# Performance work log

Measured on AMD Instinct MI355X. Metric: run time of the kernel, lower is better.

## Reference

```python
import jax, jax.numpy as jnp
import numpy as np


def conv2d(x, w, b, pad):
    # NCHW conv, stride 1, symmetric padding
    out = jax.lax.conv_general_dilated(
        x, w, window_strides=(1, 1), padding=[(pad, pad), (pad, pad)],
        dimension_numbers=("NCHW", "OIHW", "NCHW"))
    return out + b[None, :, None, None]


def setup_inputs() -> dict:
    key = jax.random.key(0)
    ks = jax.random.split(key, 18)
    B, C, H, W = 4, 256, 64, 64
    Cq = C // 16  # 16
    Ck = C // 8   # 32
    s = 0.02
    return {
        "x": jax.random.normal(ks[0], (B, C, H, W), jnp.float32),
        "dw1_w": jax.random.normal(ks[1], (Cq, C, 7, 7), jnp.float32) * s,
        "dw1_b": jnp.zeros((Cq,), jnp.float32),
        "dw2_w": jax.random.normal(ks[2], (Cq, C, 11, 11), jnp.float32) * s,
        "dw2_b": jnp.zeros((Cq,), jnp.float32),
        "key_w": jax.random.normal(ks[3], (Ck, C, 1, 1), jnp.float32) * s,
        "key_b": jnp.zeros((Ck,), jnp.float32),
        "value_w": jax.random.normal(ks[4], (C, C, 1, 1), jnp.float32) * s,
        "value_b": jnp.zeros((C,), jnp.float32),
        "conv1_w": jax.random.normal(ks[5], (Cq, C, 3, 3), jnp.float32) * s,
        "conv1_b": jnp.zeros((Cq,), jnp.float32),
        "conv2_w": jax.random.normal(ks[6], (C, Cq, 3, 3), jnp.float32) * s,
        "conv2_b": jnp.zeros((C,), jnp.float32),
        "se_w": jax.random.normal(ks[7], (C, C, 1, 1), jnp.float32) * s,
        "se_b": jnp.zeros((C,), jnp.float32),
        "gamma1": jnp.zeros((1,), jnp.float32) + 0.1,  # nonzero so attention path is exercised
        "gamma2": jnp.zeros((1,), jnp.float32) + 0.1,
    }


def reference(x, dw1_w, dw1_b, dw2_w, dw2_b, key_w, key_b, value_w, value_b,
              conv1_w, conv1_b, conv2_w, conv2_b, se_w, se_b, gamma1, gamma2):
    B, C, H, W = x.shape
    HW = H * W
    # q: concat of 7x7 and 11x11 conv branches -> (B, HW, C//8)
    q = jnp.concatenate([conv2d(x, dw1_w, dw1_b, 3), conv2d(x, dw2_w, dw2_b, 5)], axis=1)
    q = q.reshape(B, -1, HW).transpose(0, 2, 1)
    # k: 1x1 conv -> (B, C//8, HW)
    k = conv2d(x, key_w, key_b, 0).reshape(B, -1, HW)
    # raw (unscaled) full spatial attention, softmax over last dim
    att = jax.nn.softmax(jnp.einsum("bnc,bcm->bnm", q, k), axis=-1)  # (B, HW, HW)
    v = conv2d(x, value_w, value_b, 0).reshape(B, C, HW)
    out = jnp.einsum("bcm,bnm->bcn", v, att).reshape(B, C, H, W)
    # local conv branch + channel attention (SE)
    y = conv2d(jax.nn.silu(conv2d(x, conv1_w, conv1_b, 1)), conv2_w, conv2_b, 1)
    pooled = jnp.mean(y, axis=(2, 3), keepdims=True)  # (B, C, 1, 1)
    se = y * jax.nn.sigmoid(conv2d(pooled, se_w, se_b, 0))
    return gamma1 * out + gamma2 * se + x
```

## Files before the change

kernel.cpp:

```cpp
#include <hip/hip_runtime.h>

typedef unsigned short u16;
typedef __bf16 bf16x8 __attribute__((ext_vector_type(8)));
typedef float f32x4 __attribute__((ext_vector_type(4)));
typedef float f32x16 __attribute__((ext_vector_type(16)));

#define MFMA16(A,B,C) __builtin_amdgcn_mfma_f32_16x16x32_bf16((A),(B),(C),0,0,0)
#define MFMA32(A,B,C) __builtin_amdgcn_mfma_f32_32x32x16_bf16((A),(B),(C),0,0,0)

__device__ __forceinline__ u16 f2b(float f){
  union { float f; unsigned u; } X; X.f = f;
  unsigned r = X.u + 0x7FFFu + ((X.u >> 16) & 1u);
  return (u16)(r >> 16);
}
__device__ __forceinline__ float b2f(u16 h){
  union { unsigned u; float f; } X; X.u = ((unsigned)h) << 16; return X.f;
}
__device__ __forceinline__ u16 f2b_trunc(float f){
  union { float f; unsigned u; } X; X.f = f;
  return (u16)(X.u >> 16);
}
__device__ __forceinline__ bf16x8 ld_frag(const u16* p){
  union { uint4 u; bf16x8 v; } U; U.u = *(const uint4*)p; return U.v;
}

__global__ __launch_bounds__(256) void k_prep_w(
    const float* __restrict__ dw1, const float* __restrict__ dw2,
    const float* __restrict__ cw1, const float* __restrict__ kw,
    const float* __restrict__ vw,  const float* __restrict__ cw2,
    u16* __restrict__ wB, u16* __restrict__ wC,
    u16* __restrict__ kwt, u16* __restrict__ vwt, u16* __restrict__ w2t){
  int i = blockIdx.x * 256 + threadIdx.x;
  const int NB = 991232, NC = 73728, NK = 8192, NV = 65536, N2 = 40960;
  if(i < NB){
    int tap = i >> 13, rem = i & 8191;
    int chunk = rem >> 9, r2 = rem & 511;
    int oc = r2 >> 4, ci = chunk*16 + (r2 & 15);
    int dy = tap / 11, dx = tap - dy*11;
    float v;
    if(oc < 16){
      v = (dy >= 2 && dy <= 8 && dx >= 2 && dx <= 8) ? dw1[(oc*256 + ci)*49 + (dy-2)*7 + (dx-2)] : 0.f;
    } else {
      v = dw2[((oc-16)*256 + ci)*121 + tap];
    }
    wB[i] = f2b(v);
    return;
  }
  i -= NB;
  if(i < NC){
    int tap = i >> 13, rem = i & 8191;
    int chunk = rem >> 9, r2 = rem & 511;
    int oc = r2 >> 4, ci = chunk*16 + (r2 & 15);
    wC[i] = (oc < 16) ? f2b(cw1[(oc*256 + ci)*9 + tap]) : (u16)0;
    return;
  }
  i -= NC;
  if(i < NK){ kwt[i] = f2b(kw[i]); return; }
  i -= NK;
  if(i < NV){ vwt[i] = f2b(vw[i]); return; }
  i -= NV;
  if(i < N2){
    int co = i/160, kk = i - co*160;
    int tap = kk >> 4, ci = kk & 15;
    w2t[i] = (tap < 9) ? f2b(cw2[co*144 + ci*9 + tap]) : (u16)0;
    return;
  }
}

__global__ __launch_bounds__(256) void k_prep_x(const float* __restrict__ x, u16* __restrict__ xp){
  __shared__ float tile[32][33];
  const int bid = blockIdx.x;
  const int b = bid >> 10, rem = bid & 1023;
  const int c0 = (rem >> 7) << 5, m0 = (rem & 127) << 5;
  const int t = threadIdx.x;
  { const int cg = t >> 5, mm = t & 31;
    #pragma unroll
    for(int i=0;i<4;i++)
      tile[cg*4+i][mm] = x[((size_t)(b*256 + c0 + cg*4 + i) << 12) + m0 + mm];
  }
  __syncthreads();
  { const int cp = (t & 15) << 1, mloc = t >> 4;
    #pragma unroll
    for(int half = 0; half < 2; ++half){
      const int ml = half*16 + mloc;
      const int m = m0 + ml;
      const int yy = (m >> 6) + 5, xx = (m & 63) + 5;
      const int ci = c0 + cp;
      const int chunk = ci >> 4, wi = ci & 15;
      u16 lo = f2b(tile[cp][ml]), hi = f2b(tile[cp+1][ml]);
      *(unsigned*)&xp[(((size_t)(b*16 + chunk)*74 + yy)*80 + xx)*16 + wi] = ((unsigned)hi << 16) | lo;
    }
  }
}

__global__ __launch_bounds__(256) void k_qconv(
    const u16* __restrict__ xp, const u16* __restrict__ wB, const u16* __restrict__ wC,
    u16* __restrict__ qp){
  __shared__ __align__(16) u16 buf[15360];
  const int bid = blockIdx.x;
  const int rg = bid & 31, b = (bid >> 5) & 3, kq = bid >> 7;
  const int y0 = rg << 1;
  const int t = threadIdx.x, wv = t >> 6, lane = t & 63;
  const int m = lane & 31, kh = lane >> 5;
  const int laneoff = m*16 + kh*8;
  const int r = wv & 1, xo = (wv >> 1) << 5;
  const f32x16 z16 = {0.f,0.f,0.f,0.f,0.f,0.f,0.f,0.f,0.f,0.f,0.f,0.f,0.f,0.f,0.f,0.f};
  f32x16 acc = z16, acc1 = z16;

  #pragma unroll 1
  for(int c = 0; c < 2; ++c){
    const int chunk = kq*2 + c;
    const uint4* src = (const uint4*)(xp + ((size_t)((b*16 + chunk)*74 + y0))*1280);
    __syncthreads();
    for(int e = t; e < 1920; e += 256){
      ((uint4*)buf)[(e & 1)*960 + (e >> 1)] = src[e];
    }
    __syncthreads();
    const u16* wBc = wB + chunk*512 + laneoff;
    const u16* wCc = wC + chunk*512 + laneoff;
    const u16* ap = buf + kh*7680 + (r*80 + xo + m)*8;
    #pragma unroll 1
    for(int dy = 0; dy < 11; ++dy){
      const u16* rowp = ap + dy*640;
      const u16* wrow = wBc + dy*11*8192;
      const bool in1y = (dy >= 4) & (dy <= 6);
      #pragma unroll
      for(int dx = 0; dx < 11; ++dx){
        bf16x8 A = ld_frag(rowp + dx*8);
        bf16x8 B = ld_frag(wrow + dx*8192);
        acc = MFMA32(A, B, acc);
        if(in1y && dx >= 4 && dx <= 6){
          bf16x8 B1 = ld_frag(wCc + ((dy-4)*3 + (dx-4))*8192);
          acc1 = MFMA32(A, B1, acc1);
        }
      }
    }
  }

  u16* qb = qp + ((size_t)kq*16384 + (b << 12) + (y0 + r)*64 + xo) * 48;
  #pragma unroll
  for(int reg = 0; reg < 16; ++reg){
    const int row = (reg & 3) + ((reg >> 2) << 3) + (kh << 2);
    qb[row*48 + m] = f2b(acc[reg]);
    if(m < 16) qb[row*48 + 32 + m] = f2b(acc1[reg]);
  }
}

__global__ __launch_bounds__(256) void k_qfin(
    const u16* __restrict__ qp, const float* __restrict__ b7,
    const float* __restrict__ b11, const float* __restrict__ b1,
    u16* __restrict__ q_t, u16* __restrict__ t1){
  const int t = threadIdx.x, wv = t >> 6, lane = t & 63;
  const int px = blockIdx.x*4 + wv;
  if(lane >= 48) return;
  const size_t off = (size_t)px*48 + lane;
  float s = 0.f;
  #pragma unroll
  for(int sp = 0; sp < 8; ++sp) s += b2f(qp[off + (size_t)sp*786432]);
  const float LOG2E = 1.44269504f;
  if(lane < 16){
    q_t[px*32 + lane] = f2b((s + b7[lane]) * LOG2E);
  } else if(lane < 32){
    q_t[px*32 + lane] = f2b((s + b11[lane - 16]) * LOG2E);
  } else {
    float v = s + b1[lane - 32];
    t1[px*16 + lane - 32] = f2b(v / (1.f + __expf(-v)));
  }
}

__global__ __launch_bounds__(256) void k_kv(
    const u16* __restrict__ xp, const u16* __restrict__ vwt, const u16* __restrict__ kwt,
    const float* __restrict__ vb, const float* __restrict__ kb,
    u16* __restrict__ vt, u16* __restrict__ k_t){
  const int bid = blockIdx.x;
  const int h = bid & 3, blk = (bid >> 2) & 63, b = bid >> 8;
  const int wv = threadIdx.x >> 6, lane = threadIdx.x & 63;
  const int col = lane & 15, quad = lane >> 4;
  const int m0 = (blk << 6) + (wv << 4);
  f32x4 z = {0.f,0.f,0.f,0.f};
  f32x4 av[4], ak[2];
  #pragma unroll
  for(int i=0;i<4;i++) av[i] = z;
  ak[0] = z; ak[1] = z;
  const int m = m0 + col;
  const int py = (m >> 6) + 5, pxx = (m & 63) + 5;
  #pragma unroll 1
  for(int ch = 0; ch < 8; ++ch){
    const int cio = ch*32 + quad*8;
    const int chunk = cio >> 4, wi = cio & 15;
    bf16x8 xf = ld_frag(xp + (((size_t)(b*16 + chunk)*74 + py)*80 + pxx)*16 + wi);
    #pragma unroll
    for(int ct2 = 0; ct2 < 4; ++ct2){
      bf16x8 wf = ld_frag(vwt + (((h*4 + ct2)*16 + col) << 8) + cio);
      av[ct2] = MFMA16(wf, xf, av[ct2]);
    }
    if(h == 0){
      #pragma unroll
      for(int kt = 0; kt < 2; ++kt){
        bf16x8 kf = ld_frag(kwt + ((kt*16 + col) << 8) + cio);
        ak[kt] = MFMA16(xf, kf, ak[kt]);
      }
    }
  }
  const int g = m0 >> 5, lo = (m0 & 31) + col;
  #pragma unroll
  for(int ct2 = 0; ct2 < 4; ++ct2){
    #pragma unroll
    for(int r = 0; r < 4; ++r){
      const int c = (h*4 + ct2)*16 + quad*4 + r;
      vt[((size_t)(b*128 + g)*256 + c)*32 + lo] = f2b(av[ct2][r] + vb[c]);
    }
  }
  if(h == 0){
    #pragma unroll
    for(int kt = 0; kt < 2; ++kt){
      #pragma unroll
      for(int r = 0; r < 4; ++r){
        const int mq = b*4096 + m0 + quad*4 + r;
        k_t[mq*32 + kt*16 + col] = f2b((ak[kt][r] + kb[kt*16 + col]) );
      }
    }
  }
}

__global__ __launch_bounds__(512) void k_attn(
    const u16* __restrict__ q_t, const u16* __restrict__ k_t,
    const u16* __restrict__ vt, u16* __restrict__ Op,
    float* __restrict__ lsav){
  __shared__ __align__(16) u16 P[2][128][72];
  __shared__ float lred[2][128];
  __shared__ float l_l[128];
  const int bid = blockIdx.x;
  const int q0 = (bid & 31) << 7, b = (bid >> 5) & 3, ks = bid >> 7;
  const int t = threadIdx.x, wv = t >> 6, lane = t & 63, col = lane & 15, quad = lane >> 4;
  const int qp2 = wv & 3, kh2 = wv >> 2;
  const int cb = wv << 5;
  const bf16x8 qf0 = ld_frag(q_t + (size_t)(b*4096 + q0 + (qp2*2+0)*16 + col) * 32 + quad*8);
  const bf16x8 qf1 = ld_frag(q_t + (size_t)(b*4096 + q0 + (qp2*2+1)*16 + col) * 32 + quad*8);
  const f32x4 z = {0.f,0.f,0.f,0.f};
  f32x4 acc[8][2];
  #pragma unroll
  for(int qq=0;qq<8;qq++){ acc[qq][0] = z; acc[qq][1] = z; }
  float lp0[4] = {0.f,0.f,0.f,0.f};
  float lp1[4] = {0.f,0.f,0.f,0.f};
  const u16* kbase = k_t + (size_t)(b*4096) * 32;
  const u16* vbase = vt + (size_t)(b*128) * 8192;

  const int ktEnd = ks*16 + 16;
  for(int kt = ks*16; kt < ktEnd; ++kt){
    const int pb = kt & 1;
    const int mm0 = kt << 6;
    {
      #pragma unroll
      for(int ki = 0; ki < 2; ++ki){
        bf16x8 kf = ld_frag(kbase + (size_t)(mm0 + (kh2*2+ki)*16 + col) * 32 + quad*8);
        f32x4 s0 = MFMA16(qf0, kf, z);
        f32x4 s1 = MFMA16(qf1, kf, z);
        const int cc = (kh2*2+ki)*16 + col;
        u16* P0 = &P[pb][(qp2*2+0)*16 + quad*4][cc];
        u16* P1 = &P[pb][(qp2*2+1)*16 + quad*4][cc];
        #pragma unroll
        for(int r = 0; r < 4; ++r){
          float p0 = exp2f(s0[r]); lp0[r] += p0; P0[r*72] = f2b_trunc(p0);
          float p1 = exp2f(s1[r]); lp1[r] += p1; P1[r*72] = f2b_trunc(p1);
        }
      }
    }
    __syncthreads();
    {
      bf16x8 vf[2][2];
      #pragma unroll
      for(int ct = 0; ct < 2; ++ct)
        #pragma unroll
        for(int chh = 0; chh < 2; ++chh)
          vf[ct][chh] = ld_frag(vbase + ((size_t)(kt*2 + chh)*256 + cb + ct*16 + col)*32 + quad*8);
      #pragma unroll
      for(int qq = 0; qq < 8; ++qq){
        bf16x8 pa0 = ld_frag(&P[pb][qq*16 + col][quad*8]);
        bf16x8 pa1 = ld_frag(&P[pb][qq*16 + col][32 + quad*8]);
        acc[qq][0] = MFMA16(pa0, vf[0][0], acc[qq][0]);
        acc[qq][1] = MFMA16(pa0, vf[1][0], acc[qq][1]);
        acc[qq][0] = MFMA16(pa1, vf[0][1], acc[qq][0]);
        acc[qq][1] = MFMA16(pa1, vf[1][1], acc[qq][1]);
      }
    }
  }
  #pragma unroll
  for(int r = 0; r < 4; ++r){
    lp0[r] += __shfl_xor(lp0[r],1); lp0[r] += __shfl_xor(lp0[r],2);
    lp0[r] += __shfl_xor(lp0[r],4); lp0[r] += __shfl_xor(lp0[r],8);
    lp1[r] += __shfl_xor(lp1[r],1); lp1[r] += __shfl_xor(lp1[r],2);
    lp1[r] += __shfl_xor(lp1[r],4); lp1[r] += __shfl_xor(lp1[r],8);
  }
  if(col == 0){
    #pragma unroll
    for(int r = 0; r < 4; ++r){
      lred[kh2][(qp2*2+0)*16 + quad*4 + r] = lp0[r];
      lred[kh2][(qp2*2+1)*16 + quad*4 + r] = lp1[r];
    }
  }
  __syncthreads();
  if(t < 128){
    const float L = lred[0][t] + lred[1][t];
    l_l[t] = L;
    lsav[ks*16384 + b*4096 + q0 + t] = L;
  }
  __syncthreads();
  #pragma unroll
  for(int qq = 0; qq < 8; ++qq){
    #pragma unroll
    for(int r = 0; r < 4; ++r){
      const float inv = 1.f / l_l[qq*16 + quad*4 + r];
      const int n = q0 + qq*16 + quad*4 + r;
      u16* orow = Op + ((size_t)(ks*16384 + b*4096 + n) << 8) + cb + col;
      orow[0]  = f2b(acc[qq][0][r] * inv);
      orow[16] = f2b(acc[qq][1][r] * inv);
    }
  }
}

__global__ __launch_bounds__(256) void k_conv2(
    const u16* __restrict__ t1, const u16* __restrict__ w2t, const float* __restrict__ b2,
    u16* __restrict__ y_t, float* __restrict__ pooled){
  __shared__ __align__(16) u16 im[64][168];
  __shared__ float pool_l[64];
  const int bid = blockIdx.x;
  const int h = bid & 3, y = (bid >> 2) & 63, b = bid >> 8;
  const int t = threadIdx.x;
  if(t < 64) pool_l[t] = 0.f;
  const u16* t1b = t1 + ((size_t)(b*4096) << 4);
  { const int px = t >> 2, ci0 = (t & 3) << 2;
    #pragma unroll
    for(int tap = 0; tap < 9; ++tap){
      const int ky = (tap*11) >> 5, kx = tap - ky*3;
      const int ryy = y + ky - 1, rxx = px + kx - 1;
      uint2 val = make_uint2(0u, 0u);
      if((unsigned)ryy < 64u && (unsigned)rxx < 64u)
        val = *(const uint2*)(t1b + (((ryy << 6) + rxx) << 4) + ci0);
      *(uint2*)&im[px][tap*16 + ci0] = val;
    }
    for(int e = t; e < 1024; e += 256){ im[e >> 4][144 + (e & 15)] = 0; }
  }
  __syncthreads();
  const int wv = t >> 6, lane = t & 63, col = lane & 15, quad = lane >> 4;
  const f32x4 z = {0.f,0.f,0.f,0.f};
  f32x4 acc[4];
  #pragma unroll
  for(int i=0;i<4;i++) acc[i] = z;
  #pragma unroll
  for(int ch = 0; ch < 5; ++ch){
    bf16x8 af = ld_frag(&im[wv*16 + col][ch*32 + quad*8]);
    #pragma unroll
    for(int j = 0; j < 4; ++j){
      bf16x8 wf = ld_frag(w2t + ((h*4 + j)*16 + col)*160 + ch*32 + quad*8);
      acc[j] = MFMA16(af, wf, acc[j]);
    }
  }
  const int m0 = (y << 6) + (wv << 4) + (quad << 2);
  #pragma unroll
  for(int j = 0; j < 4; ++j){
    const int c = (h*4 + j)*16 + col;
    const float bias = b2[c];
    float s = 0.f;
    #pragma unroll
    for(int r = 0; r < 4; ++r){
      float v = acc[j][r] + bias;
      y_t[((size_t)(b*4096 + m0 + r) << 8) + c] = f2b(v);
      s += v;
    }
    s += __shfl_xor(s, 16); s += __shfl_xor(s, 32);
    if(quad == 0) atomicAdd(&pool_l[c - h*64], s);
  }
  __syncthreads();
  if(t < 64) atomicAdd(&pooled[b*256 + h*64 + t], pool_l[t]);
}

__global__ __launch_bounds__(256) void k_final(
    const u16* __restrict__ Op, const u16* __restrict__ y_t, const float* __restrict__ x,
    const float* __restrict__ lsav, const float* __restrict__ pooled,
    const float* __restrict__ sew, const float* __restrict__ seb,
    const float* __restrict__ g1p, const float* __restrict__ g2p,
    float* __restrict__ out){
  __shared__ float tO[32][65];
  __shared__ float tY[32][65];
  __shared__ float gate_l[32];
  const int bid = blockIdx.x;
  const int b = bid >> 9, rem = bid & 511;
  const int c0 = (rem >> 6) << 5, m0 = (rem & 63) << 6;
  const int t = threadIdx.x;
  const float g1 = g1p[0], g2 = g2p[0];
  { const int cl = t >> 3, k0 = (t & 7) << 5;
    const int c = c0 + cl;
    const float* wr = sew + (size_t)c*256 + k0;
    const float* pr = pooled + b*256 + k0;
    float part = 0.f;
    #pragma unroll
    for(int j = 0; j < 32; j += 4){
      float4 w4 = *(const float4*)(wr + j);
      float4 p4 = *(const float4*)(pr + j);
      part += w4.x*p4.x + w4.y*p4.y + w4.z*p4.z + w4.w*p4.w;
    }
    part += __shfl_xor(part, 1); part += __shfl_xor(part, 2); part += __shfl_xor(part, 4);
    if((t & 7) == 0){
      float a = part * (1.f/4096.f) + seb[c];
      gate_l[cl] = g2 / (1.f + __expf(-a));
    }
  }
  { const int ml = t >> 2, cg = (t & 3) << 3;
    const int gq = b*4096 + m0 + ml;
    const float l0 = lsav[gq], l1 = lsav[16384 + gq], l2 = lsav[32768 + gq], l3 = lsav[49152 + gq];
    const float inv = 1.f / (l0 + l1 + l2 + l3);
    const float w0 = l0*inv, w1 = l1*inv, w2 = l2*inv, w3 = l3*inv;
    const size_t base = ((size_t)gq << 8) + c0 + cg;
    union { uint4 u; u16 s[8]; } A0, A1, A2, A3;
    A0.u = *(const uint4*)(Op + base);
    A1.u = *(const uint4*)(Op + base + ((size_t)16384 << 8));
    A2.u = *(const uint4*)(Op + base + ((size_t)32768 << 8));
    A3.u = *(const uint4*)(Op + base + ((size_t)49152 << 8));
    #pragma unroll
    for(int i = 0; i < 8; ++i)
      tO[cg+i][ml] = w0*b2f(A0.s[i]) + w1*b2f(A1.s[i]) + w2*b2f(A2.s[i]) + w3*b2f(A3.s[i]);
    const u16* yrow = y_t + base;
    uint4 yu = *(const uint4*)yrow;
    tY[cg+0][ml]=b2f((u16)(yu.x & 0xffffu)); tY[cg+1][ml]=b2f((u16)(yu.x >> 16));
    tY[cg+2][ml]=b2f((u16)(yu.y & 0xffffu)); tY[cg+3][ml]=b2f((u16)(yu.y >> 16));
    tY[cg+4][ml]=b2f((u16)(yu.z & 0xffffu)); tY[cg+5][ml]=b2f((u16)(yu.z >> 16));
    tY[cg+6][ml]=b2f((u16)(yu.w & 0xffffu)); tY[cg+7][ml]=b2f((u16)(yu.w >> 16));
  }
  __syncthreads();
  { const int cl = t >> 3, mg = (t & 7) << 3;
    const int c = c0 + cl;
    const float gate = gate_l[cl];
    const float* xrow = x + ((size_t)(b*256 + c) << 12) + m0 + mg;
    float* orow = out + ((size_t)(b*256 + c) << 12) + m0 + mg;
    float4 x0 = *(const float4*)xrow, x1 = *(const float4*)(xrow + 4);
    float4 r0, r1;
    r0.x = g1*tO[cl][mg+0] + gate*tY[cl][mg+0] + x0.x;
    r0.y = g1*tO[cl][mg+1] + gate*tY[cl][mg+1] + x0.y;
    r0.z = g1*tO[cl][mg+2] + gate*tY[cl][mg+2] + x0.z;
    r0.w = g1*tO[cl][mg+3] + gate*tY[cl][mg+3] + x0.w;
    r1.x = g1*tO[cl][mg+4] + gate*tY[cl][mg+4] + x1.x;
    r1.y = g1*tO[cl][mg+5] + gate*tY[cl][mg+5] + x1.y;
    r1.z = g1*tO[cl][mg+6] + gate*tY[cl][mg+6] + x1.z;
    r1.w = g1*tO[cl][mg+7] + gate*tY[cl][mg+7] + x1.w;
    *(float4*)orow = r0;
    *(float4*)(orow + 4) = r1;
  }
}

extern "C" void kernel_launch(void* const* d_in, const int* in_sizes, int n_in,
                              void* d_out, int out_size, void* d_ws, size_t ws_size,
                              hipStream_t stream){
  (void)in_sizes; (void)n_in; (void)out_size; (void)ws_size;
  const float* x    = (const float*)d_in[0];
  const float* dw1w = (const float*)d_in[1];
  const float* dw1b = (const float*)d_in[2];
  const float* dw2w = (const float*)d_in[3];
  const float* dw2b = (const float*)d_in[4];
  const float* keyw = (const float*)d_in[5];
  const float* keyb = (const float*)d_in[6];
  const float* valw = (const float*)d_in[7];
  const float* valb = (const float*)d_in[8];
  const float* c1w  = (const float*)d_in[9];
  const float* c1b  = (const float*)d_in[10];
  const float* c2w  = (const float*)d_in[11];
  const float* c2b  = (const float*)d_in[12];
  const float* sew  = (const float*)d_in[13];
  const float* seb  = (const float*)d_in[14];
  const float* g1   = (const float*)d_in[15];
  const float* g2   = (const float*)d_in[16];
  float* out = (float*)d_out;

  char* w = (char*)d_ws;
  auto take = [&](size_t bytes) -> char* {
    char* p = w; w += (bytes + 255) & ~(size_t)255; return p;
  };
  u16*  Op   = (u16*)  take(33554432);
  u16*  q_t  = (u16*)  take(1048576);
  u16*  k_t  = (u16*)  take(1048576);
  u16*  vt   = (u16*)  take(8388608);
  u16*  t1   = (u16*)  take(524288);
  u16*  y_t  = (u16*)  take(8388608);
  u16*  kwt  = (u16*)  take(16384);
  u16*  vwt  = (u16*)  take(131072);
  u16*  w2t  = (u16*)  take(81920);
  float* pooled = (float*)take(4096);
  float* lsav   = (float*)take(262144);

  u16*  xp = Op;
  u16*  qp = Op + 6062080;
  u16*  wB = vt;
  u16*  wC = vt + 991232;

  hipMemsetAsync(xp, 0, 12124160, stream);
  hipMemsetAsync(pooled, 0, 4096, stream);
  k_prep_w<<<4608, 256, 0, stream>>>(dw1w, dw2w, c1w, keyw, valw, c2w, wB, wC, kwt, vwt, w2t);
  k_prep_x<<<4096, 256, 0, stream>>>(x, xp);
  k_qconv<<<1024, 256, 0, stream>>>(xp, wB, wC, qp);
  k_qfin<<<4096, 256, 0, stream>>>(qp, dw1b, dw2b, c1b, q_t, t1);
  k_kv<<<1024, 256, 0, stream>>>(xp, vwt, kwt, valb, keyb, vt, k_t);
  k_attn<<<512, 512, 0, stream>>>(q_t, k_t, vt, Op, lsav);
  k_conv2<<<1024, 256, 0, stream>>>(t1, w2t, c2b, y_t, pooled);
  k_final<<<2048, 256, 0, stream>>>(Op, y_t, x, lsav, pooled, sew, seb, g1, g2, out);
}
```

Baseline: 281.7 us.

## Restructure attention kernel: register-resident P via permlane swap, async LDS V staging

Rewrites the attention kernel to compute S^T with 32x32 MFMAs so the exponentiated scores stay in registers. They are converted with packed bf16 conversion and lane-swapped with permlane32_swap into A-operand layout, which removes the P round trip through shared memory and one barrier per tile. V tiles are double-buffered into swizzled LDS using global_load_lds async copies. Each wave now owns 32 queries by 128 channels, and the row-sum reduction is simplified to a single shuffle. This adds LDS pressure (64KB) and register pressure from four f32x16 accumulators, and it relies on gfx950-specific intrinsics.

```diff
diff --git a/kernel.cpp b/kernel.cpp
--- a/kernel.cpp
+++ b/kernel.cpp
@@ -1,6 +1,7 @@
 #include <hip/hip_runtime.h>
 
 typedef unsigned short u16;
+typedef unsigned u32;
 typedef __bf16 bf16x8 __attribute__((ext_vector_type(8)));
 typedef float f32x4 __attribute__((ext_vector_type(4)));
 typedef float f32x16 __attribute__((ext_vector_type(16)));
@@ -22,6 +23,18 @@
 }
 __device__ __forceinline__ bf16x8 ld_frag(const u16* p){
   union { uint4 u; bf16x8 v; } U; U.u = *(const uint4*)p; return U.v;
+}
+__device__ __forceinline__ u32 pkbf(float a, float b){
+  u32 r; asm("v_cvt_pk_bf16_f32 %0, %1, %2" : "=v"(r) : "v"(a), "v"(b)); return r;
+}
+__device__ __forceinline__ void pl32swap(u32& x, u32& y){
+  auto r = __builtin_amdgcn_permlane32_swap(x, y, false, false);
+  x = r[0]; y = r[1];
+}
+__device__ __forceinline__ void gld16(const u16* g, u16* l){
+  __builtin_amdgcn_global_load_lds(
+      (const __attribute__((address_space(1))) u32*)g,
+      (__attribute__((address_space(3))) u32*)l, 16, 0, 0);
 }
 
 __global__ __launch_bounds__(256) void k_prep_w(
@@ -223,99 +236,98 @@
   }
 }
 
-__global__ __launch_bounds__(512) void k_attn(
+__global__ __launch_bounds__(512, 4) void k_attn(
     const u16* __restrict__ q_t, const u16* __restrict__ k_t,
     const u16* __restrict__ vt, u16* __restrict__ Op,
     float* __restrict__ lsav){
-  __shared__ __align__(16) u16 P[2][128][72];
-  __shared__ float lred[2][128];
-  __shared__ float l_l[128];
+  __shared__ __align__(16) u16 V[2][16384];
   const int bid = blockIdx.x;
   const int q0 = (bid & 31) << 7, b = (bid >> 5) & 3, ks = bid >> 7;
-  const int t = threadIdx.x, wv = t >> 6, lane = t & 63, col = lane & 15, quad = lane >> 4;
-  const int qp2 = wv & 3, kh2 = wv >> 2;
-  const int cb = wv << 5;
-  const bf16x8 qf0 = ld_frag(q_t + (size_t)(b*4096 + q0 + (qp2*2+0)*16 + col) * 32 + quad*8);
-  const bf16x8 qf1 = ld_frag(q_t + (size_t)(b*4096 + q0 + (qp2*2+1)*16 + col) * 32 + quad*8);
-  const f32x4 z = {0.f,0.f,0.f,0.f};
-  f32x4 acc[8][2];
-  #pragma unroll
-  for(int qq=0;qq<8;qq++){ acc[qq][0] = z; acc[qq][1] = z; }
-  float lp0[4] = {0.f,0.f,0.f,0.f};
-  float lp1[4] = {0.f,0.f,0.f,0.f};
-  const u16* kbase = k_t + (size_t)(b*4096) * 32;
-  const u16* vbase = vt + (size_t)(b*128) * 8192;
-
-  const int ktEnd = ks*16 + 16;
-  for(int kt = ks*16; kt < ktEnd; ++kt){
-    const int pb = kt & 1;
-    const int mm0 = kt << 6;
-    {
+  const int t = threadIdx.x, wv = t >> 6, lane = t & 63;
+  const int cq = lane & 31, hi = lane >> 5;
+  const int wq = wv >> 1, ch = wv & 1;
+  const int swz = (cq & 7) << 4;
+  const int cbase = (ch*128 + cq) * 128;
+
+  const u16* qrow = q_t + ((size_t)(b*4096 + q0 + wq*32 + cq) << 5) + hi*8;
+  const bf16x8 qf0 = ld_frag(qrow), qf1 = ld_frag(qrow + 16);
+  const u16* kbase = k_t + ((size_t)(b*4096 + ks*1024 + cq) << 5) + hi*8;
+  const u16* vsrc = vt + ((size_t)(b*128 + ks*32) << 13);
+
+  u32 srcoff[4];
+  #pragma unroll
+  for(int s = 0; s < 4; ++s){
+    const int idx = s*512 + t;
+    const int c = idx >> 3;
+    const int rs = ((idx & 7) << 4) ^ ((c & 7) << 4);
+    srcoff[s] = ((rs >> 6) << 13) + (c << 5) + ((rs & 63) >> 1);
+  }
+
+  const f32x16 z16 = {0.f,0.f,0.f,0.f,0.f,0.f,0.f,0.f,0.f,0.f,0.f,0.f,0.f,0.f,0.f,0.f};
+  f32x16 acc0 = z16, acc1 = z16, acc2 = z16, acc3 = z16;
+  float lsum = 0.f;
+
+  #pragma unroll
+  for(int s = 0; s < 4; ++s)
+    gld16(vsrc + srcoff[s], &V[0][s*4096 + (wv << 9)]);
+  __syncthreads();
+
+  #pragma unroll 1
+  for(int it = 0; it < 16; ++it){
+    const int cur = it & 1;
+    if(it < 15){
+      const u16* gb = vsrc + ((size_t)(it + 1) << 14);
       #pragma unroll
-      for(int ki = 0; ki < 2; ++ki){
-        bf16x8 kf = ld_frag(kbase + (size_t)(mm0 + (kh2*2+ki)*16 + col) * 32 + quad*8);
-        f32x4 s0 = MFMA16(qf0, kf, z);
-        f32x4 s1 = MFMA16(qf1, kf, z);
-        const int cc = (kh2*2+ki)*16 + col;
-        u16* P0 = &P[pb][(qp2*2+0)*16 + quad*4][cc];
-        u16* P1 = &P[pb][(qp2*2+1)*16 + quad*4][cc];
-        #pragma unroll
-        for(int r = 0; r < 4; ++r){
-          float p0 = exp2f(s0[r]); lp0[r] += p0; P0[r*72] = f2b_trunc(p0);
-          float p1 = exp2f(s1[r]); lp1[r] += p1; P1[r*72] = f2b_trunc(p1);
-        }
-      }
+      for(int s = 0; s < 4; ++s)
+        gld16(gb + srcoff[s], &V[cur ^ 1][s*4096 + (wv << 9)]);
+    }
+    const u16* kp = kbase + ((size_t)it << 11);
+    const u16* Vb = &V[cur][0];
+    #pragma unroll
+    for(int sub = 0; sub < 2; ++sub){
+      const bf16x8 kf0 = ld_frag(kp + sub*1024);
+      const bf16x8 kf1 = ld_frag(kp + sub*1024 + 16);
+      f32x16 S = MFMA32(kf0, qf0, z16);
+      S = MFMA32(kf1, qf1, S);
+      #pragma unroll
+      for(int rr = 0; rr < 16; ++rr){ S[rr] = exp2f(S[rr]); lsum += S[rr]; }
+      u32 a0 = pkbf(S[0], S[1]),   b0 = pkbf(S[4], S[5]);
+      u32 a1 = pkbf(S[2], S[3]),   b1 = pkbf(S[6], S[7]);
+      u32 c0 = pkbf(S[8], S[9]),   d0 = pkbf(S[12], S[13]);
+      u32 c1 = pkbf(S[10], S[11]), d1 = pkbf(S[14], S[15]);
+      pl32swap(a0, b0); pl32swap(a1, b1); pl32swap(c0, d0); pl32swap(c1, d1);
+      union { u32 w[4]; bf16x8 v; } A0, A1;
+      A0.w[0] = a0; A0.w[1] = a1; A0.w[2] = b0; A0.w[3] = b1;
+      A1.w[0] = c0; A1.w[1] = c1; A1.w[2] = d0; A1.w[3] = d1;
+      const int o0 = cbase + ((((sub << 6) | (hi << 4))) ^ swz);
+      const char* vb0 = (const char*)Vb + o0;
+      const char* vb1 = (const char*)Vb + (o0 ^ 32);
+      acc0 = MFMA32(A0.v, ld_frag((const u16*)(vb0)),         acc0);
+      acc1 = MFMA32(A0.v, ld_frag((const u16*)(vb0 + 4096)),  acc1);
+      acc2 = MFMA32(A0.v, ld_frag((const u16*)(vb0 + 8192)),  acc2);
+      acc3 = MFMA32(A0.v, ld_frag((const u16*)(vb0 + 12288)), acc3);
+      acc0 = MFMA32(A1.v, ld_frag((const u16*)(vb1)),         acc0);
+      acc1 = MFMA32(A1.v, ld_frag((const u16*)(vb1 + 4096)),  acc1);
+      acc2 = MFMA32(A1.v, ld_frag((const u16*)(vb1 + 8192)),  acc2);
+      acc3 = MFMA32(A1.v, ld_frag((const u16*)(vb1 + 12288)), acc3);
     }
     __syncthreads();
-    {
-      bf16x8 vf[2][2];
-      #pragma unroll
-      for(int ct = 0; ct < 2; ++ct)
-        #pragma unroll
-        for(int chh = 0; chh < 2; ++chh)
-          vf[ct][chh] = ld_frag(vbase + ((size_t)(kt*2 + chh)*256 + cb + ct*16 + col)*32 + quad*8);
-      #pragma unroll
-      for(int qq = 0; qq < 8; ++qq){
-        bf16x8 pa0 = ld_frag(&P[pb][qq*16 + col][quad*8]);
-        bf16x8 pa1 = ld_frag(&P[pb][qq*16 + col][32 + quad*8]);
-        acc[qq][0] = MFMA16(pa0, vf[0][0], acc[qq][0]);
-        acc[qq][1] = MFMA16(pa0, vf[1][0], acc[qq][1]);
-        acc[qq][0] = MFMA16(pa1, vf[0][1], acc[qq][0]);
-        acc[qq][1] = MFMA16(pa1, vf[1][1], acc[qq][1]);
-      }
-    }
-  }
-  #pragma unroll
-  for(int r = 0; r < 4; ++r){
-    lp0[r] += __shfl_xor(lp0[r],1); lp0[r] += __shfl_xor(lp0[r],2);
-    lp0[r] += __shfl_xor(lp0[r],4); lp0[r] += __shfl_xor(lp0[r],8);
-    lp1[r] += __shfl_xor(lp1[r],1); lp1[r] += __shfl_xor(lp1[r],2);
-    lp1[r] += __shfl_xor(lp1[r],4); lp1[r] += __shfl_xor(lp1[r],8);
-  }
-  if(col == 0){
-    #pragma unroll
-    for(int r = 0; r < 4; ++r){
-      lred[kh2][(qp2*2+0)*16 + quad*4 + r] = lp0[r];
-      lred[kh2][(qp2*2+1)*16 + quad*4 + r] = lp1[r];
-    }
-  }
-  __syncthreads();
-  if(t < 128){
-    const float L = lred[0][t] + lred[1][t];
-    l_l[t] = L;
-    lsav[ks*16384 + b*4096 + q0 + t] = L;
-  }
-  __syncthreads();
-  #pragma unroll
-  for(int qq = 0; qq < 8; ++qq){
-    #pragma unroll
-    for(int r = 0; r < 4; ++r){
-      const float inv = 1.f / l_l[qq*16 + quad*4 + r];
-      const int n = q0 + qq*16 + quad*4 + r;
-      u16* orow = Op + ((size_t)(ks*16384 + b*4096 + n) << 8) + cb + col;
-      orow[0]  = f2b(acc[qq][0][r] * inv);
-      orow[16] = f2b(acc[qq][1][r] * inv);
-    }
+  }
+
+  lsum += __shfl_xor(lsum, 32);
+  const float invl = 1.f / lsum;
+  if(ch == 0 && hi == 0)
+    lsav[ks*16384 + b*4096 + q0 + wq*32 + cq] = lsum;
+  u16* ob = Op + (((size_t)(ks*16384 + b*4096 + q0 + wq*32)) << 8) + ch*128 + cq;
+  #pragma unroll
+  for(int reg = 0; reg < 16; ++reg){
+    const int row = (reg & 3) + ((reg >> 2) << 3) + (hi << 2);
+    const float inv = __shfl(invl, row);
+    u16* orow = ob + ((size_t)row << 8);
+    orow[0]  = f2b(acc0[reg] * inv);
+    orow[32] = f2b(acc1[reg] * inv);
+    orow[64] = f2b(acc2[reg] * inv);
+    orow[96] = f2b(acc3[reg] * inv);
   }
 }
 
```

Result: slower. 292.1 us (+3.7%).
